# Kernel tuning notes

Hardware: AMD Instinct MI355X
Metric: run time of the kernel (lower is better)

Reference implementation:

```python
import jax, jax.numpy as jnp
import numpy as np

D_MODEL = 1024
N_HEADS = 16
D_K = D_MODEL // N_HEADS
THETA = 10000.0
B, S = 2, 2048


def _rope(x):
    # x: [B, H, S, Dh], interleaved-pair RoPE with positions arange(S)
    Dh = x.shape[-1]
    inv_freq = 1.0 / (THETA ** (jnp.arange(0, Dh, 2, dtype=jnp.float32) / Dh))  # [Dh/2]
    pos = jnp.arange(x.shape[-2], dtype=jnp.float32)
    ang = pos[:, None] * inv_freq[None, :]                      # [S, Dh/2]
    cos = jnp.repeat(jnp.cos(ang), 2, axis=-1).astype(x.dtype)  # [S, Dh]
    sin = jnp.repeat(jnp.sin(ang), 2, axis=-1).astype(x.dtype)
    # rotate pairs: (x_2k, x_2k+1) -> (-x_2k+1, x_2k)
    xp = x.reshape(*x.shape[:-1], Dh // 2, 2)
    rot = jnp.stack((-xp[..., 1], xp[..., 0]), axis=-1).reshape(x.shape)
    return x * cos + rot * sin


def setup_inputs() -> dict:
    key = jax.random.key(0)
    ks = jax.random.split(key, 5)
    std = (2.0 / (D_MODEL + D_MODEL)) ** 0.5
    return {
        "x": jax.random.normal(ks[0], (B, S, D_MODEL), dtype=jnp.float32),
        "wq": jax.random.normal(ks[1], (D_MODEL, D_MODEL), dtype=jnp.float32) * std,
        "wk": jax.random.normal(ks[2], (D_MODEL, D_MODEL), dtype=jnp.float32) * std,
        "wv": jax.random.normal(ks[3], (D_MODEL, D_MODEL), dtype=jnp.float32) * std,
        "wo": jax.random.normal(ks[4], (D_MODEL, D_MODEL), dtype=jnp.float32) * std,
    }


def reference(x, wq, wk, wv, wo):
    b, s, _ = x.shape
    def split_heads(t):
        return t.reshape(b, s, N_HEADS, D_K).transpose(0, 2, 1, 3)  # [B,H,S,Dk]
    # Linear: y = x @ W.T  (weights stored [out, in])
    q = split_heads(jnp.einsum('bsd,od->bso', x, wq))
    k = split_heads(jnp.einsum('bsd,od->bso', x, wk))
    v = split_heads(jnp.einsum('bsd,od->bso', x, wv))
    q = _rope(q)
    k = _rope(k)
    scores = jnp.einsum('bhqd,bhkd->bhqk', q, k) / jnp.sqrt(jnp.asarray(D_K, x.dtype))
    causal = jnp.tril(jnp.ones((s, s), dtype=bool))
    scores = jnp.where(causal[None, None], scores, -jnp.inf)
    attn = jax.nn.softmax(scores, axis=-1)
    out = jnp.einsum('bhqk,bhkd->bhqd', attn, v)
    out = out.transpose(0, 2, 1, 3).reshape(b, s, D_MODEL)
    return jnp.einsum('bsd,od->bso', out, wo)
```

## Files before the change

kernel.cpp:

```cpp
#include <hip/hip_runtime.h>


typedef unsigned short u16;
typedef __attribute__((ext_vector_type(8))) short short8;
typedef __attribute__((ext_vector_type(4))) float float4v;

typedef const __attribute__((address_space(1))) void GV;
typedef __attribute__((address_space(3))) void LV;

#define VSTR 72
#define QSCL 0.18033688011112042f

__device__ __forceinline__ u16 f2b(float f) {
    union { float f; unsigned int i; } t; t.f = f;
    unsigned int r = t.i + 0x7fffu + ((t.i >> 16) & 1u);
    return (u16)(r >> 16);
}

__global__ __launch_bounds__(256) void cvt_all(
    const float4* __restrict__ x,  const float4* __restrict__ wq,
    const float4* __restrict__ wk, const float4* __restrict__ wv,
    const float4* __restrict__ wo,
    u16* __restrict__ xb, u16* __restrict__ wcat, u16* __restrict__ wob)
{
    const int i = blockIdx.x * 256 + threadIdx.x;
    const float4* s; u16* d; int off;
    if (i < 524288) { s = x; d = xb; off = i; }
    else {
        const int widx = i - 524288;
        const int w = widx >> 17, o = widx & 131071;
        switch (w) {
            case 0:  s = wq; d = wcat;              break;
            case 1:  s = wk; d = wcat + (1 << 20);  break;
            case 2:  s = wv; d = wcat + (2 << 20);  break;
            default: s = wo; d = wob;               break;
        }
        off = o;
    }
    float4 a = s[2 * off], b = s[2 * off + 1];
    u16 t[8] = {f2b(a.x), f2b(a.y), f2b(a.z), f2b(a.w),
                f2b(b.x), f2b(b.y), f2b(b.z), f2b(b.w)};
    reinterpret_cast<int4*>(d)[off] = *reinterpret_cast<int4*>(t);
}

__global__ __launch_bounds__(256) void rope_tab(float2* __restrict__ tab) {
    const int i = blockIdx.x * 256 + threadIdx.x;
    const int pos = i >> 5, fi = i & 31;
    const float freq = exp2f((float)fi * -0.4152410118609203f);
    float sn, cs; sincosf((float)pos * freq, &sn, &cs);
    tab[i] = make_float2(cs, sn);
}

template<int NT, int ROPE, int NBLK>
__global__ __launch_bounds__(256) void gemm_tile(
    const u16* __restrict__ X, const u16* __restrict__ Wb,
    u16* __restrict__ Yq, u16* __restrict__ Yk, u16* __restrict__ Yv,
    float* __restrict__ Yf, const float2* __restrict__ tab)
{
    __shared__ u16 As[128 * 64];
    __shared__ u16 Bs[NT * 32 * 64];

    const int tid  = threadIdx.x;
    const int wave = tid >> 6;
    const int lane = tid & 63;
    const int quad = lane >> 4;
    const int l16  = lane & 15;
    const int wm = (wave >> 1) * 64, wn = (wave & 1) * (NT * 16);
    const int g = blockIdx.x;
    const int rr = g >> 3;
    const int m0 = ((g & 7) * 4 + rr / NBLK) * 128;
    const int n0 = (rr % NBLK) * (NT * 32);
    const int lrow = lane >> 3;
    const int cg8  = (lane & 7) ^ lrow;

    float4v acc[4][NT];
#pragma unroll
    for (int mt = 0; mt < 4; mt++)
#pragma unroll
        for (int nt = 0; nt < NT; nt++) acc[mt][nt] = (float4v){0.f, 0.f, 0.f, 0.f};

    for (int kb = 0; kb < 1024; kb += 64) {
        __syncthreads();
#pragma unroll
        for (int t = 0; t < 4; t++) {
            const int I = wave * 4 + t;
            const u16* gp = X + (size_t)(m0 + I * 8 + lrow) * 1024 + kb + cg8 * 8;
            __builtin_amdgcn_global_load_lds((GV*)gp, (LV*)&As[I * 512], 16, 0, 0);
        }
#pragma unroll
        for (int t = 0; t < NT; t++) {
            const int I = wave * NT + t;
            const u16* gp = Wb + (size_t)(n0 + I * 8 + lrow) * 1024 + kb + cg8 * 8;
            __builtin_amdgcn_global_load_lds((GV*)gp, (LV*)&Bs[I * 512], 16, 0, 0);
        }
        __syncthreads();
#pragma unroll
        for (int ks = 0; ks < 2; ks++) {
            const int su = ((ks * 4 + quad) ^ (l16 & 7)) * 8;
            short8 af[4], bf[NT];
#pragma unroll
            for (int t = 0; t < 4; t++)
                af[t] = *reinterpret_cast<const short8*>(&As[(wm + t * 16 + l16) * 64 + su]);
#pragma unroll
            for (int t = 0; t < NT; t++)
                bf[t] = *reinterpret_cast<const short8*>(&Bs[(wn + t * 16 + l16) * 64 + su]);
#pragma unroll
            for (int mt = 0; mt < 4; mt++)
#pragma unroll
                for (int nt = 0; nt < NT; nt++)
                    acc[mt][nt] = __builtin_amdgcn_mfma_f32_16x16x32_bf16(af[mt], bf[nt], acc[mt][nt], 0, 0, 0);
        }
    }

    if (ROPE) {
#pragma unroll
        for (int nt = 0; nt < NT; nt++) {
            const int cg = n0 + wn + nt * 16 + l16;
            const int buf = cg >> 10;
            const int c = cg & 1023;
            u16* dst = (buf == 0) ? Yq : ((buf == 1) ? Yk : Yv);
            const bool rp = (buf < 2);
            const float scl = (buf == 0) ? QSCL : 1.0f;
            const int fi = (cg & 63) >> 1;
#pragma unroll
            for (int mt = 0; mt < 4; mt++)
#pragma unroll
                for (int r = 0; r < 4; r++) {
                    const int row = m0 + wm + mt * 16 + quad * 4 + r;
                    float v = acc[mt][nt][r];
                    if (rp) {
                        const float2 t = tab[((row & 2047) << 5) + fi];
                        const float partner = __shfl_xor(v, 1);
                        v = (l16 & 1) ? fmaf(v, t.x,  partner * t.y)
                                      : fmaf(v, t.x, -partner * t.y);
                    }
                    dst[(size_t)row * 1024 + c] = f2b(v * scl);
                }
        }
    } else {
#pragma unroll
        for (int nt = 0; nt < NT; nt++) {
            const int col = n0 + wn + nt * 16 + l16;
#pragma unroll
            for (int mt = 0; mt < 4; mt++)
#pragma unroll
                for (int r = 0; r < 4; r++) {
                    const int row = m0 + wm + mt * 16 + quad * 4 + r;
                    Yf[(size_t)row * 1024 + col] = acc[mt][nt][r];
                }
        }
    }
}

__global__ __launch_bounds__(256, 2) void attn_kernel(
    const u16* Q, const u16* __restrict__ K,
    const u16* __restrict__ V, u16* O)
{
    __shared__ u16 Vt[64 * VSTR];
    __shared__ u16 Ps[8 * 16 * VSTR];

    const int tid  = threadIdx.x;
    const int wave = tid >> 6;
    const int lane = tid & 63;
    const int quad = lane >> 4;
    const int l16  = lane & 15;
    const int g = blockIdx.x;
    const int xcd = g & 7, slot = g >> 3;
    const int G = (slot >> 4) * 8 + xcd;
    const int qtA = slot & 15;
    const int qtB = 31 - qtA;
    const int b = G & 1, h = G >> 1;
    const size_t base = ((size_t)b * 2048) * 1024 + (size_t)h * 64;

    short8 qfA[2], qfB[2];
    {
        const size_t ra = base + (size_t)(qtA * 64 + wave * 16 + l16) * 1024;
        qfA[0] = *reinterpret_cast<const short8*>(Q + ra + quad * 8);
        qfA[1] = *reinterpret_cast<const short8*>(Q + ra + 32 + quad * 8);
        const size_t rb = base + (size_t)(qtB * 64 + wave * 16 + l16) * 1024;
        qfB[0] = *reinterpret_cast<const short8*>(Q + rb + quad * 8);
        qfB[1] = *reinterpret_cast<const short8*>(Q + rb + 32 + quad * 8);
    }

    float4v oA[4], oB[4];
#pragma unroll
    for (int i = 0; i < 4; i++) { oA[i] = (float4v){0.f,0.f,0.f,0.f}; oB[i] = (float4v){0.f,0.f,0.f,0.f}; }
    float sA[4] = {0.f,0.f,0.f,0.f}, sB[4] = {0.f,0.f,0.f,0.f};

    u16* PwA = Ps + wave * 16 * VSTR;
    u16* PwB = Ps + (wave + 4) * 16 * VSTR;
    const int srow = tid >> 2;
    const int cb   = (tid & 3) << 4;
    const int sxw  = srow ^ cb;

    const u16* Vp = V + base + (size_t)srow * 1024 + cb;
    const u16* kbase = K + base + (size_t)l16 * 1024 + quad * 8;
    int4 vr0 = *reinterpret_cast<const int4*>(Vp);
    int4 vr1 = *reinterpret_cast<const int4*>(Vp + 8);
    short8 kn[4][2], kc[4][2], vf[4][2];
#pragma unroll
    for (int nt = 0; nt < 4; nt++)
#pragma unroll
        for (int ks = 0; ks < 2; ks++)
            kn[nt][ks] = *reinterpret_cast<const short8*>(kbase + (size_t)(nt * 16) * 1024 + ks * 32);

    auto qk = [&](const short8 (&qf)[2], float4v (&sacc)[4]) {
#pragma unroll
        for (int nt = 0; nt < 4; nt++) {
            sacc[nt] = (float4v){0.f, 0.f, 0.f, 0.f};
#pragma unroll
            for (int ks = 0; ks < 2; ks++)
                sacc[nt] = __builtin_amdgcn_mfma_f32_16x16x32_bf16(qf[ks], kc[nt][ks], sacc[nt], 0, 0, 0);
        }
    };
    auto sm = [&](const float4v (&sacc)[4], float (&sr)[4], u16* Pw, bool diag) {
#pragma unroll
        for (int r = 0; r < 4; r++) {
            const int qloc = wave * 16 + quad * 4 + r;
#pragma unroll
            for (int nt = 0; nt < 4; nt++) {
                float sv = sacc[nt][r];
                if (diag && (nt * 16 + l16 > qloc)) sv = -1e30f;
                const float p = exp2f(sv);
                sr[r] += p;
                Pw[(quad * 4 + r) * VSTR + nt * 16 + l16] = f2b(p);
            }
        }
    };
    auto pv = [&](const u16* Pw, float4v (&oc)[4]) {
#pragma unroll
        for (int ks = 0; ks < 2; ks++) {
            short8 pf = *reinterpret_cast<const short8*>(&Pw[l16 * VSTR + ks * 32 + quad * 8]);
#pragma unroll
            for (int dt = 0; dt < 4; dt++)
                oc[dt] = __builtin_amdgcn_mfma_f32_16x16x32_bf16(pf, vf[dt][ks], oc[dt], 0, 0, 0);
        }
    };

    for (int j = 0; j <= qtB; j++) {
        __syncthreads();
        {
            const u16* a = reinterpret_cast<const u16*>(&vr0);
            const u16* c = reinterpret_cast<const u16*>(&vr1);
#pragma unroll
            for (int e = 0; e < 8; e++) Vt[(cb + e) * VSTR + sxw] = a[e];
#pragma unroll
            for (int e = 0; e < 8; e++) Vt[(cb + 8 + e) * VSTR + sxw] = c[e];
        }
#pragma unroll
        for (int nt = 0; nt < 4; nt++)
#pragma unroll
            for (int ks = 0; ks < 2; ks++) kc[nt][ks] = kn[nt][ks];
        __syncthreads();
        if (j < qtB) {
            Vp += 65536;
            vr0 = *reinterpret_cast<const int4*>(Vp);
            vr1 = *reinterpret_cast<const int4*>(Vp + 8);
            const u16* kb2 = kbase + (size_t)(j + 1) * 65536;
#pragma unroll
            for (int nt = 0; nt < 4; nt++)
#pragma unroll
                for (int ks = 0; ks < 2; ks++)
                    kn[nt][ks] = *reinterpret_cast<const short8*>(kb2 + (size_t)(nt * 16) * 1024 + ks * 32);
        }
#pragma unroll
        for (int nt = 0; nt < 4; nt++)
#pragma unroll
            for (int ks = 0; ks < 2; ks++)
                vf[nt][ks] = *reinterpret_cast<const short8*>(&Vt[(nt * 16 + l16) * VSTR + ((ks * 32 + quad * 8) ^ (nt << 4))]);

        if (j <= qtA) {
            float4v xA[4], xB[4];
            qk(qfA, xA);
            qk(qfB, xB);
            sm(xA, sA, PwA, j == qtA);
            sm(xB, sB, PwB, false);
            __builtin_amdgcn_wave_barrier();
            pv(PwA, oA);
            pv(PwB, oB);
            __builtin_amdgcn_wave_barrier();
        } else {
            float4v xB[4];
            qk(qfB, xB);
            sm(xB, sB, PwB, j == qtB);
            __builtin_amdgcn_wave_barrier();
            pv(PwB, oB);
            __builtin_amdgcn_wave_barrier();
        }
    }

#pragma unroll
    for (int r = 0; r < 4; r++) {
        float la = sA[r], lb = sB[r];
#pragma unroll
        for (int msk = 1; msk < 16; msk <<= 1) { la += __shfl_xor(la, msk); lb += __shfl_xor(lb, msk); }
        const float invA = 1.0f / la, invB = 1.0f / lb;
        const int rloc = wave * 16 + quad * 4 + r;
        const size_t rowA = base + (size_t)(qtA * 64 + rloc) * 1024;
        const size_t rowB = base + (size_t)(qtB * 64 + rloc) * 1024;
#pragma unroll
        for (int dt = 0; dt < 4; dt++) {
            O[rowA + dt * 16 + l16] = f2b(oA[dt][r] * invA);
            O[rowB + dt * 16 + l16] = f2b(oB[dt][r] * invB);
        }
    }
}

extern "C" void kernel_launch(void* const* d_in, const int* in_sizes, int n_in,
                              void* d_out, int out_size, void* d_ws, size_t ws_size,
                              hipStream_t stream) {
    (void)in_sizes; (void)n_in; (void)out_size; (void)ws_size;
    const float* x  = (const float*)d_in[0];
    const float* wq = (const float*)d_in[1];
    const float* wk = (const float*)d_in[2];
    const float* wv = (const float*)d_in[3];
    const float* wo = (const float*)d_in[4];

    const size_t MN = (size_t)4096 * 1024;

    u16* xb   = (u16*)d_out;
    u16* wcat = xb + MN;
    float2* tab = (float2*)(wcat + (size_t)3072 * 1024);
    u16* qbuf = (u16*)d_ws;
    u16* kbuf = qbuf + MN;
    u16* vbuf = kbuf + MN;
    u16* wob  = vbuf + MN;

    cvt_all<<<4096, 256, 0, stream>>>((const float4*)x, (const float4*)wq,
                                      (const float4*)wk, (const float4*)wv,
                                      (const float4*)wo, xb, wcat, wob);
    rope_tab<<<256, 256, 0, stream>>>(tab);
    gemm_tile<4, 1, 24><<<768, 256, 0, stream>>>(xb, wcat, qbuf, kbuf, vbuf, nullptr, tab);
    attn_kernel<<<512, 256, 0, stream>>>(qbuf, kbuf, vbuf, qbuf);
    gemm_tile<2, 0, 16><<<512, 256, 0, stream>>>(qbuf, wob, nullptr, nullptr, nullptr, (float*)d_out, nullptr);
}
```

Baseline: 230.8 us.

## Keep softmax probabilities in registers via transposed QK and bpermute shuffles

Swaps the MFMA operands in QK^T so each lane holds one query row's scores across keys. It converts P to bf16 with packed cvt instructions and rearranges it into the PV A-operand layout with ds_bpermute instead of round-tripping through shared memory. This removes the Ps LDS buffer, its stores, loads and wave barriers, and cuts the row-sum reduction to two cross-lane shuffles. In exchange it adds eight bpermutes and selects per block, and relies on inline asm for the bf16 packing.

```diff
diff --git a/kernel.cpp b/kernel.cpp
--- a/kernel.cpp
+++ b/kernel.cpp
@@ -157,7 +157,6 @@
     const u16* __restrict__ V, u16* O)
 {
     __shared__ u16 Vt[64 * VSTR];
-    __shared__ u16 Ps[8 * 16 * VSTR];
 
     const int tid  = threadIdx.x;
     const int wave = tid >> 6;
@@ -185,10 +184,8 @@
     float4v oA[4], oB[4];
 #pragma unroll
     for (int i = 0; i < 4; i++) { oA[i] = (float4v){0.f,0.f,0.f,0.f}; oB[i] = (float4v){0.f,0.f,0.f,0.f}; }
-    float sA[4] = {0.f,0.f,0.f,0.f}, sB[4] = {0.f,0.f,0.f,0.f};
-
-    u16* PwA = Ps + wave * 16 * VSTR;
-    u16* PwB = Ps + (wave + 4) * 16 * VSTR;
+    float sA = 0.f, sB = 0.f;
+
     const int srow = tid >> 2;
     const int cb   = (tid & 3) << 4;
     const int sxw  = srow ^ cb;
@@ -204,37 +201,57 @@
         for (int ks = 0; ks < 2; ks++)
             kn[nt][ks] = *reinterpret_cast<const short8*>(kbase + (size_t)(nt * 16) * 1024 + ks * 32);
 
+    const int bpa0 = (((quad & 1) * 2) * 16 + l16) * 4;
+    const int bpa1 = bpa0 + 64;
+    const bool hiq = quad >= 2;
+    const int qloc = wave * 16 + l16;
+
     auto qk = [&](const short8 (&qf)[2], float4v (&sacc)[4]) {
 #pragma unroll
         for (int nt = 0; nt < 4; nt++) {
             sacc[nt] = (float4v){0.f, 0.f, 0.f, 0.f};
 #pragma unroll
             for (int ks = 0; ks < 2; ks++)
-                sacc[nt] = __builtin_amdgcn_mfma_f32_16x16x32_bf16(qf[ks], kc[nt][ks], sacc[nt], 0, 0, 0);
+                sacc[nt] = __builtin_amdgcn_mfma_f32_16x16x32_bf16(kc[nt][ks], qf[ks], sacc[nt], 0, 0, 0);
         }
     };
-    auto sm = [&](const float4v (&sacc)[4], float (&sr)[4], u16* Pw, bool diag) {
-#pragma unroll
-        for (int r = 0; r < 4; r++) {
-            const int qloc = wave * 16 + quad * 4 + r;
-#pragma unroll
-            for (int nt = 0; nt < 4; nt++) {
+    auto smx = [&](const float4v (&sacc)[4], float &sr, short8 (&pa)[2], bool diag) {
+        unsigned int w[4][2];
+#pragma unroll
+        for (int nt = 0; nt < 4; nt++) {
+            float p[4];
+#pragma unroll
+            for (int r = 0; r < 4; r++) {
                 float sv = sacc[nt][r];
-                if (diag && (nt * 16 + l16 > qloc)) sv = -1e30f;
-                const float p = exp2f(sv);
-                sr[r] += p;
-                Pw[(quad * 4 + r) * VSTR + nt * 16 + l16] = f2b(p);
+                if (diag && (nt * 16 + quad * 4 + r > qloc)) sv = -1e30f;
+                p[r] = exp2f(sv);
+                sr += p[r];
             }
+            asm("v_cvt_pk_bf16_f32 %0, %1, %2" : "=v"(w[nt][0]) : "v"(p[0]), "v"(p[1]));
+            asm("v_cvt_pk_bf16_f32 %0, %1, %2" : "=v"(w[nt][1]) : "v"(p[2]), "v"(p[3]));
+        }
+#pragma unroll
+        for (int ks = 0; ks < 2; ks++) {
+            unsigned int pw[4];
+#pragma unroll
+            for (int j = 0; j < 4; j++) {
+                const int addr = (j >> 1) ? bpa1 : bpa0;
+                const int rp = j & 1;
+                int lo_ = __builtin_amdgcn_ds_bpermute(addr, (int)w[2 * ks][rp]);
+                int hi_ = __builtin_amdgcn_ds_bpermute(addr, (int)w[2 * ks + 1][rp]);
+                pw[j] = (unsigned int)(hiq ? hi_ : lo_);
+            }
+            union { unsigned int u[4]; short8 s; } t;
+            t.u[0] = pw[0]; t.u[1] = pw[1]; t.u[2] = pw[2]; t.u[3] = pw[3];
+            pa[ks] = t.s;
         }
     };
-    auto pv = [&](const u16* Pw, float4v (&oc)[4]) {
-#pragma unroll
-        for (int ks = 0; ks < 2; ks++) {
-            short8 pf = *reinterpret_cast<const short8*>(&Pw[l16 * VSTR + ks * 32 + quad * 8]);
+    auto pv = [&](const short8 (&pa)[2], float4v (&oc)[4]) {
+#pragma unroll
+        for (int ks = 0; ks < 2; ks++)
 #pragma unroll
             for (int dt = 0; dt < 4; dt++)
-                oc[dt] = __builtin_amdgcn_mfma_f32_16x16x32_bf16(pf, vf[dt][ks], oc[dt], 0, 0, 0);
-        }
+                oc[dt] = __builtin_amdgcn_mfma_f32_16x16x32_bf16(pa[ks], vf[dt][ks], oc[dt], 0, 0, 0);
     };
 
     for (int j = 0; j <= qtB; j++) {
@@ -273,31 +290,30 @@
             float4v xA[4], xB[4];
             qk(qfA, xA);
             qk(qfB, xB);
-            sm(xA, sA, PwA, j == qtA);
-            sm(xB, sB, PwB, false);
-            __builtin_amdgcn_wave_barrier();
-            pv(PwA, oA);
-            pv(PwB, oB);
-            __builtin_amdgcn_wave_barrier();
+            short8 paA[2], paB[2];
+            smx(xA, sA, paA, j == qtA);
+            smx(xB, sB, paB, false);
+            pv(paA, oA);
+            pv(paB, oB);
         } else {
             float4v xB[4];
             qk(qfB, xB);
-            sm(xB, sB, PwB, j == qtB);
-            __builtin_amdgcn_wave_barrier();
-            pv(PwB, oB);
-            __builtin_amdgcn_wave_barrier();
-        }
-    }
-
+            short8 paB[2];
+            smx(xB, sB, paB, j == qtB);
+            pv(paB, oB);
+        }
+    }
+
+    float tA = sA, tB = sB;
+    tA += __shfl_xor(tA, 16); tA += __shfl_xor(tA, 32);
+    tB += __shfl_xor(tB, 16); tB += __shfl_xor(tB, 32);
 #pragma unroll
     for (int r = 0; r < 4; r++) {
-        float la = sA[r], lb = sB[r];
-#pragma unroll
-        for (int msk = 1; msk < 16; msk <<= 1) { la += __shfl_xor(la, msk); lb += __shfl_xor(lb, msk); }
-        const float invA = 1.0f / la, invB = 1.0f / lb;
-        const int rloc = wave * 16 + quad * 4 + r;
-        const size_t rowA = base + (size_t)(qtA * 64 + rloc) * 1024;
-        const size_t rowB = base + (size_t)(qtB * 64 + rloc) * 1024;
+        const int rl = quad * 4 + r;
+        const float invA = 1.0f / __shfl(tA, rl);
+        const float invB = 1.0f / __shfl(tB, rl);
+        const size_t rowA = base + (size_t)(qtA * 64 + wave * 16 + rl) * 1024;
+        const size_t rowB = base + (size_t)(qtB * 64 + wave * 16 + rl) * 1024;
 #pragma unroll
         for (int dt = 0; dt < 4; dt++) {
             O[rowA + dt * 16 + l16] = f2b(oA[dt][r] * invA);
```

New measurement: 228.0 us. Within noise of the previous version (-1.2%).
